# Performance work log

Hardware: AMD Instinct MI355X
Metric: run time of the kernel (lower is better)

The kernel has to match this reference:

```python
import jax, jax.numpy as jnp
import numpy as np

B, S, DIM, H, HD = 4, 1024, 1280, 16, 80
SCALE = HD ** -0.5
ROPE_THETA = 10000.0


def rotate_half(x):
    x1, x2 = jnp.split(x, 2, axis=-1)
    return jnp.concatenate([-x2, x1], axis=-1)


def setup_inputs() -> dict:
    key = jax.random.key(0)
    ks = jax.random.split(key, 5)
    x = jax.random.normal(ks[0], (B, S, DIM), dtype=jnp.float32)
    Wqkv = jax.random.normal(ks[1], (DIM, 3 * DIM), dtype=jnp.float32) * 0.02
    bqkv = jax.random.normal(ks[2], (3 * DIM,), dtype=jnp.float32) * 0.01
    Wproj = jax.random.normal(ks[3], (DIM, DIM), dtype=jnp.float32) * 0.02
    bproj = jax.random.normal(ks[4], (DIM,), dtype=jnp.float32) * 0.01
    # realistic rotary tables: (S, HD) with duplicated freq halves (matches rotate_half layout)
    inv_freq = 1.0 / (ROPE_THETA ** (jnp.arange(0, HD, 2, dtype=jnp.float32) / HD))
    freqs = jnp.outer(jnp.arange(S, dtype=jnp.float32), inv_freq)  # (S, HD/2)
    emb = jnp.concatenate([freqs, freqs], axis=-1)  # (S, HD)
    rope_cos = jnp.cos(emb)
    rope_sin = jnp.sin(emb)
    return {"x": x, "rope_cos": rope_cos, "rope_sin": rope_sin,
            "Wqkv": Wqkv, "bqkv": bqkv, "Wproj": Wproj, "bproj": bproj}


def reference(x, rope_cos, rope_sin, Wqkv, bqkv, Wproj, bproj):
    b, s, d = x.shape
    qkv = (x @ Wqkv + bqkv).reshape(b, s, 3, H, HD)
    q, k, v = qkv[:, :, 0], qkv[:, :, 1], qkv[:, :, 2]  # each (b, s, H, HD)
    cos = rope_cos[None, :, None, :]  # (1, s, 1, HD)
    sin = rope_sin[None, :, None, :]
    q = q * cos + rotate_half(q) * sin
    k = k * cos + rotate_half(k) * sin
    # SDPA with all-ones mask (full attention)
    scores = jnp.einsum("bqhd,bkhd->bhqk", q, k) * SCALE
    probs = jax.nn.softmax(scores, axis=-1)
    out = jnp.einsum("bhqk,bkhd->bqhd", probs, v).reshape(b, s, d)
    return out @ Wproj + bproj
```

## Files before the change

kernel.cpp:

```cpp
#include <hip/hip_runtime.h>
#include <math.h>

#define SCALE_F 0.11180339887498949f
#define HDP 96

typedef short  short8  __attribute__((ext_vector_type(8)));
typedef short  short4v __attribute__((ext_vector_type(4)));
typedef float  f32x4   __attribute__((ext_vector_type(4)));
typedef __bf16 bf16x8  __attribute__((ext_vector_type(8)));

__device__ __forceinline__ float bf2f(short s) {
  union { unsigned u; float f; } v;
  v.u = ((unsigned)(unsigned short)s) << 16;
  return v.f;
}
__device__ __forceinline__ short f2b(float f) {
  __bf16 h = (__bf16)f;
  return __builtin_bit_cast(short, h);
}
__device__ __forceinline__ bool probe_is_bf16(const unsigned* probe) {
  return (probe[1] & 0xFFFFu) != 0u;
}
__device__ __forceinline__ float load_scalar(const void* p, int i, bool isb) {
  return isb ? bf2f(((const short*)p)[i]) : ((const float*)p)[i];
}

__device__ __forceinline__ void gload_lds16(const short* g, short* l) {
  __builtin_amdgcn_global_load_lds(
      (const __attribute__((address_space(1))) void*)g,
      (__attribute__((address_space(3))) void*)l, 16, 0, 0);
}

template <typename V>
__device__ __forceinline__ auto mfma_try(V a, V b, f32x4 c, int)
    -> decltype(__builtin_amdgcn_mfma_f32_16x16x32_bf16(a, b, c, 0, 0, 0)) {
  return __builtin_amdgcn_mfma_f32_16x16x32_bf16(a, b, c, 0, 0, 0);
}
template <typename V>
__device__ __forceinline__ f32x4 mfma_try(V a, V b, f32x4 c, long) {
  return __builtin_amdgcn_mfma_f32_16x16x32_bf16(
      __builtin_bit_cast(bf16x8, a), __builtin_bit_cast(bf16x8, b), c, 0, 0, 0);
}
__device__ __forceinline__ f32x4 MFMA(short8 a, short8 b, f32x4 c) {
  return mfma_try(a, b, c, 0);
}

__global__ __launch_bounds__(256) void cvt_x_kernel(
    const void* __restrict__ xin, short* __restrict__ xout,
    const unsigned* __restrict__ probe) {
  bool isb = probe_is_bf16(probe);
  size_t i = ((size_t)blockIdx.x * 256 + threadIdx.x) * 8;
  if (isb) {
    *(short8*)&xout[i] = *(const short8*)((const short*)xin + i);
  } else {
    const float* f = (const float*)xin + i;
    float4 a0 = *(const float4*)f;
    float4 a1 = *(const float4*)(f + 4);
    short8 sv;
    sv[0] = f2b(a0.x); sv[1] = f2b(a0.y); sv[2] = f2b(a0.z); sv[3] = f2b(a0.w);
    sv[4] = f2b(a1.x); sv[5] = f2b(a1.y); sv[6] = f2b(a1.z); sv[7] = f2b(a1.w);
    *(short8*)&xout[i] = sv;
  }
}

__global__ __launch_bounds__(256) void transpose_kernel(
    const void* __restrict__ in, short* __restrict__ out, int R, int C,
    const unsigned* __restrict__ probe) {
  bool isb = probe_is_bf16(probe);
  __shared__ float tile[32][33];
  int t = threadIdx.x;
  int bx = blockIdx.x;
  int by = blockIdx.y;
  int r = t >> 3, c4 = (t & 7) * 4;
  size_t idx = (size_t)(by * 32 + r) * C + bx * 32 + c4;
  if (isb) {
    short4v v = *(const short4v*)((const short*)in + idx);
    tile[r][c4 + 0] = bf2f(v[0]);
    tile[r][c4 + 1] = bf2f(v[1]);
    tile[r][c4 + 2] = bf2f(v[2]);
    tile[r][c4 + 3] = bf2f(v[3]);
  } else {
    float4 v = *(const float4*)((const float*)in + idx);
    tile[r][c4 + 0] = v.x;
    tile[r][c4 + 1] = v.y;
    tile[r][c4 + 2] = v.z;
    tile[r][c4 + 3] = v.w;
  }
  __syncthreads();
  int rr = t >> 3, k4 = (t & 7) * 4;
  short4v o;
  o[0] = f2b(tile[k4 + 0][rr]);
  o[1] = f2b(tile[k4 + 1][rr]);
  o[2] = f2b(tile[k4 + 2][rr]);
  o[3] = f2b(tile[k4 + 3][rr]);
  *(short4v*)&out[(size_t)(bx * 32 + rr) * R + by * 32 + k4] = o;
}

__global__ __launch_bounds__(512, 2) void gemm_qkv_kernel(
    const short* __restrict__ X, const short* __restrict__ Wt,
    const void* __restrict__ bias, const unsigned* __restrict__ probe,
    short* __restrict__ Qw, short* __restrict__ Kw, short* __restrict__ Vt) {
  const int K = 1280;
  __shared__ short Al[2][2][8192];
  __shared__ short Bl[2][2][8192];
  int t = threadIdx.x;
  int bm = blockIdx.x / 15, bn = blockIdx.x % 15;
  int m0 = bm * 256, n0 = bn * 256;
  int w = t >> 6, lane = t & 63;
  int quad = lane >> 4, l16 = lane & 15, l8 = l16 & 7;
  int arow = (w >> 2) * 64 + l16;
  int brow = (w & 3) * 32 + l16;
  int sr = t >> 3, t8s = t * 8;
  int sjs = (t & 7) ^ (sr & 7);
  int soff0 = ((quad ^ l8) * 8);
  int soff1 = (((4 + quad) ^ l8) * 8);
  f32x4 acc[2][2][4][2] = {};

#define STAGE8(PTR, R0, KOFF, LP)                                            \
  {                                                                          \
    const short* g_ = (PTR) + (size_t)((R0) + sr) * 1280 + (KOFF) + sjs * 8; \
    gload_lds16(g_, (LP) + t8s);                                             \
    gload_lds16(g_ + 64 * 1280, (LP) + t8s + 4096);                          \
  }

#define PHASE(S, HA, HB, QM, QN, STAGE_CODE, DO_VW)                          \
  {                                                                          \
    short8 af[4][2], bfv[2][2];                                              \
    _Pragma("unroll") for (int mt = 0; mt < 4; mt++) {                       \
      int rp_ = (arow + mt * 16) * 64;                                       \
      af[mt][0] = *(const short8*)&Al[S][HA][rp_ + soff0];                   \
      af[mt][1] = *(const short8*)&Al[S][HA][rp_ + soff1];                   \
    }                                                                        \
    _Pragma("unroll") for (int nt = 0; nt < 2; nt++) {                       \
      int rp_ = (brow + nt * 16) * 64;                                       \
      bfv[nt][0] = *(const short8*)&Bl[S][HB][rp_ + soff0];                  \
      bfv[nt][1] = *(const short8*)&Bl[S][HB][rp_ + soff1];                  \
    }                                                                        \
    STAGE_CODE;                                                              \
    asm volatile("s_waitcnt lgkmcnt(0)" ::: "memory");                       \
    __builtin_amdgcn_sched_barrier(0);                                       \
    __builtin_amdgcn_s_setprio(1);                                           \
    _Pragma("unroll") for (int mt = 0; mt < 4; mt++)                         \
      _Pragma("unroll") for (int nt = 0; nt < 2; nt++) {                     \
        acc[QM][QN][mt][nt] = MFMA(af[mt][0], bfv[nt][0], acc[QM][QN][mt][nt]); \
        acc[QM][QN][mt][nt] = MFMA(af[mt][1], bfv[nt][1], acc[QM][QN][mt][nt]); \
      }                                                                      \
    __builtin_amdgcn_s_setprio(0);                                           \
    if (DO_VW) {                                                             \
      asm volatile("s_waitcnt vmcnt(4)" ::: "memory");                       \
      __builtin_amdgcn_sched_barrier(0);                                     \
    }                                                                        \
    __builtin_amdgcn_s_barrier();                                            \
  }

  STAGE8(X,  m0,       0,  &Al[0][0][0]);
  STAGE8(X,  m0 + 128, 0,  &Al[0][1][0]);
  STAGE8(Wt, n0,       0,  &Bl[0][0][0]);
  STAGE8(Wt, n0 + 128, 0,  &Bl[0][1][0]);
  STAGE8(X,  m0,       64, &Al[1][0][0]);
  STAGE8(Wt, n0,       64, &Bl[1][0][0]);
  asm volatile("s_waitcnt vmcnt(4)" ::: "memory");
  __builtin_amdgcn_sched_barrier(0);
  __builtin_amdgcn_s_barrier();

  for (int i = 0; i < 10; i++) {
    int k1 = (2 * i + 1) * 64;
    int k2 = (2 * i + 2) * 64; if (k2 >= K) k2 = 0;
    int k3 = (2 * i + 3) * 64; if (k3 >= K) k3 = 0;
    PHASE(0, 0, 0, 0, 0, STAGE8(X,  m0 + 128, k1, &Al[1][1][0]), 0);
    PHASE(0, 0, 1, 0, 1, STAGE8(Wt, n0 + 128, k1, &Bl[1][1][0]), 0);
    PHASE(0, 1, 0, 1, 0, STAGE8(X,  m0,       k2, &Al[0][0][0]), 0);
    PHASE(0, 1, 1, 1, 1, STAGE8(Wt, n0,       k2, &Bl[0][0][0]), 1);
    PHASE(1, 0, 0, 0, 0, STAGE8(X,  m0 + 128, k2, &Al[0][1][0]), 0);
    PHASE(1, 0, 1, 0, 1, STAGE8(Wt, n0 + 128, k2, &Bl[0][1][0]), 0);
    PHASE(1, 1, 0, 1, 0, STAGE8(X,  m0,       k3, &Al[1][0][0]), 0);
    PHASE(1, 1, 1, 1, 1, STAGE8(Wt, n0,       k3, &Bl[1][0][0]), 1);
  }
  asm volatile("s_waitcnt vmcnt(0)" ::: "memory");
  __builtin_amdgcn_sched_barrier(0);

  bool isb = probe_is_bf16(probe);
  float bv[2][2];
#pragma unroll
  for (int qn = 0; qn < 2; qn++)
#pragma unroll
    for (int nt = 0; nt < 2; nt++)
      bv[qn][nt] =
          load_scalar(bias, n0 + qn * 128 + (w & 3) * 32 + nt * 16 + l16, isb);
#pragma unroll
  for (int qm = 0; qm < 2; qm++)
#pragma unroll
    for (int mt = 0; mt < 4; mt++) {
      int mbase = m0 + qm * 128 + (w >> 2) * 64 + mt * 16 + quad * 4;
      int b = mbase >> 10, sbase = mbase & 1023;
#pragma unroll
      for (int qn = 0; qn < 2; qn++)
#pragma unroll
        for (int nt = 0; nt < 2; nt++) {
          int n = n0 + qn * 128 + (w & 3) * 32 + nt * 16 + l16;
          int which = n / 1280;
          int rmod = n - which * 1280;
          int h = rmod / 80;
          int d = rmod - h * 80;
          int bh = b * 16 + h;
          if (which == 2) {
            short4v vv;
#pragma unroll
            for (int reg = 0; reg < 4; reg++)
              vv[reg] = f2b(acc[qm][qn][mt][nt][reg] + bv[qn][nt]);
            *(short4v*)&Vt[((size_t)bh * 80 + d) * 1024 + sbase] = vv;
          } else {
            short* dst = (which == 0 ? Qw : Kw);
#pragma unroll
            for (int reg = 0; reg < 4; reg++)
              dst[((size_t)bh * 1024 + sbase + reg) * HDP + d] =
                  f2b(acc[qm][qn][mt][nt][reg] + bv[qn][nt]);
          }
        }
    }
#undef PHASE
#undef STAGE8
}

__global__ __launch_bounds__(256) void rope_kernel(
    short* __restrict__ Qw, short* __restrict__ Kw,
    const void* __restrict__ cosb, const void* __restrict__ sinb,
    const unsigned* __restrict__ probe) {
  bool isb = probe_is_bf16(probe);
  int t = threadIdx.x;
  int w = t >> 6, lane = t & 63;
  int job = blockIdx.x * 4 + w;
  int which = job & 1;
  int row = job >> 1;
  int s = row & 1023;
  short* ptr = (which ? Kw : Qw) + (size_t)row * HDP;
  float scale = which ? 1.0f : SCALE_F;
  if (lane < 40) {
    float p0 = bf2f(ptr[lane]);
    float p1 = bf2f(ptr[lane + 40]);
    float c0 = load_scalar(cosb, s * 80 + lane, isb);
    float s0 = load_scalar(sinb, s * 80 + lane, isb);
    float c1 = load_scalar(cosb, s * 80 + lane + 40, isb);
    float s1 = load_scalar(sinb, s * 80 + lane + 40, isb);
    ptr[lane] = f2b((p0 * c0 - p1 * s0) * scale);
    ptr[lane + 40] = f2b((p1 * c1 + p0 * s1) * scale);
  } else if (lane < 56) {
    ptr[40 + lane] = 0;
  }
}

__global__ __launch_bounds__(512, 4) void attn_kernel(
    const short* __restrict__ Qw, const short* __restrict__ Kw,
    const short* __restrict__ Vt, short* __restrict__ out) {
  __shared__ short Klds[2][64 * 104];
  __shared__ short Vlds[2][80 * 72];
  __shared__ short Ps[8][16 * 72];
  int t = threadIdx.x;
  int w = t >> 6, lane = t & 63;
  int quad = lane >> 4, l16 = lane & 15;
  int bh = blockIdx.x & 63;
  int qt = blockIdx.x >> 6;
  int q0 = qt * 128;
  const short* Kb = Kw + (size_t)bh * 1024 * HDP;
  const short* Vb = Vt + (size_t)bh * 80 * 1024;

  short8 aq[3];
  {
    const short* qrow = Qw + ((size_t)bh * 1024 + q0 + w * 16 + l16) * HDP;
#pragma unroll
    for (int ks = 0; ks < 3; ks++)
      aq[ks] = *(const short8*)&qrow[ks * 32 + quad * 8];
  }

  short8 kreg[2], vreg[2];
#define PREFETCH(c)                                                        \
  {                                                                        \
    {                                                                      \
      int row = t / 12, col = (t % 12) * 8;                                \
      kreg[0] = *(const short8*)&Kb[(size_t)((c) + row) * HDP + col];      \
    }                                                                      \
    if (t < 256) {                                                         \
      int idx = 512 + t;                                                   \
      int row = idx / 12, col = (idx % 12) * 8;                            \
      kreg[1] = *(const short8*)&Kb[(size_t)((c) + row) * HDP + col];      \
    }                                                                      \
    {                                                                      \
      int d = t >> 3, s0 = (t & 7) * 8;                                    \
      vreg[0] = *(const short8*)&Vb[(size_t)d * 1024 + (c) + s0];          \
    }                                                                      \
    if (t < 128) {                                                         \
      int idx = 512 + t;                                                   \
      int d = idx >> 3, s0 = (idx & 7) * 8;                                \
      vreg[1] = *(const short8*)&Vb[(size_t)d * 1024 + (c) + s0];          \
    }                                                                      \
  }
#define STORE_LDS(P)                                                       \
  {                                                                        \
    {                                                                      \
      int row = t / 12, col = (t % 12) * 8;                                \
      *(short8*)&Klds[P][row * 104 + col] = kreg[0];                       \
    }                                                                      \
    if (t < 256) {                                                         \
      int idx = 512 + t;                                                   \
      int row = idx / 12, col = (idx % 12) * 8;                            \
      *(short8*)&Klds[P][row * 104 + col] = kreg[1];                       \
    }                                                                      \
    {                                                                      \
      int d = t >> 3, s0 = (t & 7) * 8;                                    \
      *(short8*)&Vlds[P][d * 72 + s0] = vreg[0];                           \
    }                                                                      \
    if (t < 128) {                                                         \
      int idx = 512 + t;                                                   \
      int d = idx >> 3, s0 = (idx & 7) * 8;                                \
      *(short8*)&Vlds[P][d * 72 + s0] = vreg[1];                           \
    }                                                                      \
  }

  PREFETCH(0);
  STORE_LDS(0);
  __syncthreads();

  f32x4 ofr[5] = {};
  float lsum[4] = {0.f, 0.f, 0.f, 0.f};
  short* Pw = &Ps[w][0];

  int p = 0;
  for (int c = 0; c < 1024; c += 64, p ^= 1) {
    if (c + 64 < 1024) PREFETCH(c + 64);
    const short* Kl = &Klds[p][0];
    const short* Vl = &Vlds[p][0];
    f32x4 sf[4] = {};
#pragma unroll
    for (int nt = 0; nt < 4; nt++) {
      short8 bk0 = *(const short8*)&Kl[(nt * 16 + l16) * 104 + 0 * 32 + quad * 8];
      short8 bk1 = *(const short8*)&Kl[(nt * 16 + l16) * 104 + 1 * 32 + quad * 8];
      short8 bk2 = *(const short8*)&Kl[(nt * 16 + l16) * 104 + 2 * 32 + quad * 8];
      sf[nt] = MFMA(aq[0], bk0, sf[nt]);
      sf[nt] = MFMA(aq[1], bk1, sf[nt]);
      sf[nt] = MFMA(aq[2], bk2, sf[nt]);
    }
#pragma unroll
    for (int r = 0; r < 4; r++) {
      float p0 = __expf(fminf(sf[0][r], 30.f));
      float p1 = __expf(fminf(sf[1][r], 30.f));
      float p2 = __expf(fminf(sf[2][r], 30.f));
      float p3 = __expf(fminf(sf[3][r], 30.f));
      sf[0][r] = p0; sf[1][r] = p1; sf[2][r] = p2; sf[3][r] = p3;
      lsum[r] += (p0 + p1) + (p2 + p3);
    }
#pragma unroll
    for (int nt = 0; nt < 4; nt++)
#pragma unroll
      for (int r = 0; r < 4; r++)
        Pw[(quad * 4 + r) * 72 + nt * 16 + l16] = f2b(sf[nt][r]);
    __threadfence_block();
    short8 ap[2];
#pragma unroll
    for (int ks = 0; ks < 2; ks++)
      ap[ks] = *(const short8*)&Pw[l16 * 72 + ks * 32 + quad * 8];
#pragma unroll
    for (int nt = 0; nt < 5; nt++) {
      short8 bv0 = *(const short8*)&Vl[(nt * 16 + l16) * 72 + 0 * 32 + quad * 8];
      short8 bv1 = *(const short8*)&Vl[(nt * 16 + l16) * 72 + 1 * 32 + quad * 8];
      ofr[nt] = MFMA(ap[0], bv0, ofr[nt]);
      ofr[nt] = MFMA(ap[1], bv1, ofr[nt]);
    }
    if (c + 64 < 1024) {
      STORE_LDS(p ^ 1);
      __syncthreads();
    }
  }
#pragma unroll
  for (int off = 1; off < 16; off <<= 1)
#pragma unroll
    for (int r = 0; r < 4; r++) lsum[r] += __shfl_xor(lsum[r], off);
  float inv[4];
#pragma unroll
  for (int r = 0; r < 4; r++) inv[r] = 1.f / lsum[r];
  int b = bh >> 4, h = bh & 15;
#pragma unroll
  for (int nt = 0; nt < 5; nt++) {
    int d = nt * 16 + l16;
#pragma unroll
    for (int r = 0; r < 4; r++) {
      int s = q0 + w * 16 + quad * 4 + r;
      out[((size_t)(b * 1024 + s)) * 1280 + h * 80 + d] = f2b(ofr[nt][r] * inv[r]);
    }
  }
}

__global__ __launch_bounds__(256) void gemm_proj_kernel(
    const short* __restrict__ A, const short* __restrict__ Wt,
    const void* __restrict__ bias, const unsigned* __restrict__ probe,
    float* __restrict__ out) {
  const int K = 1280;
  __shared__ short As[2][128 * 32];
  __shared__ short Bs[2][128 * 32];
  int t = threadIdx.x;
  int bm = blockIdx.x / 10;
  int bn = blockIdx.x % 10;
  int m0 = bm * 128, n0 = bn * 128;
  int w = t >> 6, lane = t & 63;
  int wm = w & 1, wn = w >> 1;
  int quad = lane >> 4, l16 = lane & 15;
  int row = t >> 2, ch = (t & 3) * 8, row2 = row + 64;
  int t8 = t * 8;
  const short* Ar  = A  + (size_t)(m0 + row)  * K + ch;
  const short* Ar2 = A  + (size_t)(m0 + row2) * K + ch;
  const short* Wr  = Wt + (size_t)(n0 + row)  * K + ch;
  const short* Wr2 = Wt + (size_t)(n0 + row2) * K + ch;
  f32x4 acc[4][4] = {};
  gload_lds16(Ar,  &As[0][t8]);
  gload_lds16(Ar2, &As[0][t8 + 2048]);
  gload_lds16(Wr,  &Bs[0][t8]);
  gload_lds16(Wr2, &Bs[0][t8 + 2048]);
  __syncthreads();
  int p = 0;
#define PROJ_COMPUTE(pp)                                                      \
  {                                                                           \
    short8 af[4], bfr[4];                                                     \
    _Pragma("unroll") for (int mt = 0; mt < 4; mt++)                          \
        af[mt] = *(const short8*)&As[pp][(wm * 64 + mt * 16 + l16) * 32 + quad * 8]; \
    _Pragma("unroll") for (int nt = 0; nt < 4; nt++)                          \
        bfr[nt] = *(const short8*)&Bs[pp][(wn * 64 + nt * 16 + l16) * 32 + quad * 8]; \
    _Pragma("unroll") for (int mt = 0; mt < 4; mt++)                          \
        _Pragma("unroll") for (int nt = 0; nt < 4; nt++)                      \
            acc[mt][nt] = MFMA(af[mt], bfr[nt], acc[mt][nt]);                 \
  }
  for (int k0 = 32; k0 < K; k0 += 32, p ^= 1) {
    gload_lds16(Ar + k0,  &As[p ^ 1][t8]);
    gload_lds16(Ar2 + k0, &As[p ^ 1][t8 + 2048]);
    gload_lds16(Wr + k0,  &Bs[p ^ 1][t8]);
    gload_lds16(Wr2 + k0, &Bs[p ^ 1][t8 + 2048]);
    PROJ_COMPUTE(p);
    __syncthreads();
  }
  PROJ_COMPUTE(p);
  bool isb = probe_is_bf16(probe);
  float bv[4];
#pragma unroll
  for (int nt = 0; nt < 4; nt++)
    bv[nt] = load_scalar(bias, n0 + wn * 64 + nt * 16 + l16, isb);
#pragma unroll
  for (int mt = 0; mt < 4; mt++) {
#pragma unroll
    for (int nt = 0; nt < 4; nt++) {
      int n = n0 + wn * 64 + nt * 16 + l16;
#pragma unroll
      for (int reg = 0; reg < 4; reg++) {
        int m = m0 + wm * 64 + mt * 16 + quad * 4 + reg;
        out[(size_t)m * 1280 + n] = acc[mt][nt][reg] + bv[nt];
      }
    }
  }
}

extern "C" void kernel_launch(void* const* d_in, const int* in_sizes, int n_in,
                              void* d_out, int out_size, void* d_ws, size_t ws_size,
                              hipStream_t stream) {
  const void* x        = d_in[0];
  const void* rope_cos = d_in[1];
  const void* rope_sin = d_in[2];
  const void* Wqkv     = d_in[3];
  const void* bqkv     = d_in[4];
  const void* Wproj    = d_in[5];
  const void* bproj    = d_in[6];
  const unsigned* probe = (const unsigned*)rope_cos;
  char* ws = (char*)d_ws;
  short* Wt1 = (short*)(ws + 0);
  short* Wt2 = (short*)(ws + 9830400);
  short* Qw  = (short*)(ws + 13107200);
  short* Kw  = (short*)(ws + 25690112);
  short* Vt  = (short*)(ws + 38273024);
  short* Xb  = (short*)(ws + 48758784);
  short* At  = (short*)(ws + 48758784);

  cvt_x_kernel<<<2560, 256, 0, stream>>>(x, Xb, probe);
  transpose_kernel<<<dim3(3840 / 32, 1280 / 32), 256, 0, stream>>>(Wqkv, Wt1, 1280, 3840, probe);
  transpose_kernel<<<dim3(1280 / 32, 1280 / 32), 256, 0, stream>>>(Wproj, Wt2, 1280, 1280, probe);
  gemm_qkv_kernel<<<240, 512, 0, stream>>>(Xb, Wt1, bqkv, probe, Qw, Kw, Vt);
  rope_kernel<<<32768, 256, 0, stream>>>(Qw, Kw, rope_cos, rope_sin, probe);
  attn_kernel<<<512, 512, 0, stream>>>(Qw, Kw, Vt, At);
  gemm_proj_kernel<<<32 * 10, 256, 0, stream>>>(At, Wt2, bproj, probe, (float*)d_out);
}
```

Baseline: 242.7 us.

## Restructure QKV GEMM into 4-stage k32 pipeline with 128x64 warp tiles

Replaces the quadrant-phased double-buffered K=64 main loop of the QKV GEMM with a 4-deep ring of K=32 stages. Each iteration prefetches three tiles ahead, and each warp computes a contiguous 128x64 sub-tile with 32 MFMAs per barrier. The aim is fewer barriers per MFMA and deeper latency hiding of global loads into LDS. It also changes the LDS swizzle and the warp-to-output mapping. The trade-off is less work between barriers per K-step and a different LDS access pattern, which may raise bank conflicts.

```diff
diff --git a/kernel.cpp b/kernel.cpp
--- a/kernel.cpp
+++ b/kernel.cpp
@@ -100,126 +100,102 @@
     const short* __restrict__ X, const short* __restrict__ Wt,
     const void* __restrict__ bias, const unsigned* __restrict__ probe,
     short* __restrict__ Qw, short* __restrict__ Kw, short* __restrict__ Vt) {
-  const int K = 1280;
-  __shared__ short Al[2][2][8192];
-  __shared__ short Bl[2][2][8192];
+  __shared__ short Asl[4][8192];
+  __shared__ short Bsl[4][8192];
   int t = threadIdx.x;
   int bm = blockIdx.x / 15, bn = blockIdx.x % 15;
   int m0 = bm * 256, n0 = bn * 256;
   int w = t >> 6, lane = t & 63;
-  int quad = lane >> 4, l16 = lane & 15, l8 = l16 & 7;
-  int arow = (w >> 2) * 64 + l16;
-  int brow = (w & 3) * 32 + l16;
-  int sr = t >> 3, t8s = t * 8;
-  int sjs = (t & 7) ^ (sr & 7);
-  int soff0 = ((quad ^ l8) * 8);
-  int soff1 = (((4 + quad) ^ l8) * 8);
-  f32x4 acc[2][2][4][2] = {};
-
-#define STAGE8(PTR, R0, KOFF, LP)                                            \
+  int quad = lane >> 4, l16 = lane & 15;
+  int wm = w >> 2, wn = w & 3;
+  int arow = wm * 128 + l16;
+  int brow = wn * 64 + l16;
+  int qsw8 = (quad ^ ((l16 >> 1) & 3)) * 8;
+  int srow = t >> 2, t8s = t * 8;
+  int sks = (t & 3) ^ ((srow >> 1) & 3);
+  f32x4 acc[8][4] = {};
+
+#define STAGE32(KT)                                                          \
   {                                                                          \
-    const short* g_ = (PTR) + (size_t)((R0) + sr) * 1280 + (KOFF) + sjs * 8; \
-    gload_lds16(g_, (LP) + t8s);                                             \
-    gload_lds16(g_ + 64 * 1280, (LP) + t8s + 4096);                          \
-  }
-
-#define PHASE(S, HA, HB, QM, QN, STAGE_CODE, DO_VW)                          \
-  {                                                                          \
-    short8 af[4][2], bfv[2][2];                                              \
-    _Pragma("unroll") for (int mt = 0; mt < 4; mt++) {                       \
-      int rp_ = (arow + mt * 16) * 64;                                       \
-      af[mt][0] = *(const short8*)&Al[S][HA][rp_ + soff0];                   \
-      af[mt][1] = *(const short8*)&Al[S][HA][rp_ + soff1];                   \
-    }                                                                        \
-    _Pragma("unroll") for (int nt = 0; nt < 2; nt++) {                       \
-      int rp_ = (brow + nt * 16) * 64;                                       \
-      bfv[nt][0] = *(const short8*)&Bl[S][HB][rp_ + soff0];                  \
-      bfv[nt][1] = *(const short8*)&Bl[S][HB][rp_ + soff1];                  \
-    }                                                                        \
-    STAGE_CODE;                                                              \
-    asm volatile("s_waitcnt lgkmcnt(0)" ::: "memory");                       \
-    __builtin_amdgcn_sched_barrier(0);                                       \
-    __builtin_amdgcn_s_setprio(1);                                           \
-    _Pragma("unroll") for (int mt = 0; mt < 4; mt++)                         \
-      _Pragma("unroll") for (int nt = 0; nt < 2; nt++) {                     \
-        acc[QM][QN][mt][nt] = MFMA(af[mt][0], bfv[nt][0], acc[QM][QN][mt][nt]); \
-        acc[QM][QN][mt][nt] = MFMA(af[mt][1], bfv[nt][1], acc[QM][QN][mt][nt]); \
-      }                                                                      \
-    __builtin_amdgcn_s_setprio(0);                                           \
-    if (DO_VW) {                                                             \
-      asm volatile("s_waitcnt vmcnt(4)" ::: "memory");                       \
-      __builtin_amdgcn_sched_barrier(0);                                     \
-    }                                                                        \
-    __builtin_amdgcn_s_barrier();                                            \
-  }
-
-  STAGE8(X,  m0,       0,  &Al[0][0][0]);
-  STAGE8(X,  m0 + 128, 0,  &Al[0][1][0]);
-  STAGE8(Wt, n0,       0,  &Bl[0][0][0]);
-  STAGE8(Wt, n0 + 128, 0,  &Bl[0][1][0]);
-  STAGE8(X,  m0,       64, &Al[1][0][0]);
-  STAGE8(Wt, n0,       64, &Bl[1][0][0]);
-  asm volatile("s_waitcnt vmcnt(4)" ::: "memory");
+    int kn_ = (KT);                                                          \
+    int koff_ = (kn_ < 40) ? kn_ * 32 : 0;         \
+    int Sd_ = kn_ & 3;                                                       \
+    const short* ga_ = X + (size_t)(m0 + srow) * 1280 + koff_ + sks * 8;     \
+    gload_lds16(ga_, &Asl[Sd_][t8s]);                                        \
+    gload_lds16(ga_ + 128 * 1280, &Asl[Sd_][t8s + 4096]);                    \
+    const short* gb_ = Wt + (size_t)(n0 + srow) * 1280 + koff_ + sks * 8;    \
+    gload_lds16(gb_, &Bsl[Sd_][t8s]);                                        \
+    gload_lds16(gb_ + 128 * 1280, &Bsl[Sd_][t8s + 4096]);                    \
+  }
+
+  STAGE32(0);
+  STAGE32(1);
+  STAGE32(2);
+  asm volatile("s_waitcnt vmcnt(8)" ::: "memory");
   __builtin_amdgcn_sched_barrier(0);
   __builtin_amdgcn_s_barrier();
 
-  for (int i = 0; i < 10; i++) {
-    int k1 = (2 * i + 1) * 64;
-    int k2 = (2 * i + 2) * 64; if (k2 >= K) k2 = 0;
-    int k3 = (2 * i + 3) * 64; if (k3 >= K) k3 = 0;
-    PHASE(0, 0, 0, 0, 0, STAGE8(X,  m0 + 128, k1, &Al[1][1][0]), 0);
-    PHASE(0, 0, 1, 0, 1, STAGE8(Wt, n0 + 128, k1, &Bl[1][1][0]), 0);
-    PHASE(0, 1, 0, 1, 0, STAGE8(X,  m0,       k2, &Al[0][0][0]), 0);
-    PHASE(0, 1, 1, 1, 1, STAGE8(Wt, n0,       k2, &Bl[0][0][0]), 1);
-    PHASE(1, 0, 0, 0, 0, STAGE8(X,  m0 + 128, k2, &Al[0][1][0]), 0);
-    PHASE(1, 0, 1, 0, 1, STAGE8(Wt, n0 + 128, k2, &Bl[0][1][0]), 0);
-    PHASE(1, 1, 0, 1, 0, STAGE8(X,  m0,       k3, &Al[1][0][0]), 0);
-    PHASE(1, 1, 1, 1, 1, STAGE8(Wt, n0,       k3, &Bl[1][0][0]), 1);
+  for (int kt = 0; kt < 40; kt++) {
+    int S = kt & 3;
+    const short* As = &Asl[S][0];
+    const short* Bs = &Bsl[S][0];
+    STAGE32(kt + 3);
+    short8 af[8], bfv[4];
+#pragma unroll
+    for (int mt = 0; mt < 8; mt++)
+      af[mt] = *(const short8*)&As[(arow + mt * 16) * 32 + qsw8];
+#pragma unroll
+    for (int nt = 0; nt < 4; nt++)
+      bfv[nt] = *(const short8*)&Bs[(brow + nt * 16) * 32 + qsw8];
+    asm volatile("s_waitcnt lgkmcnt(0)" ::: "memory");
+    __builtin_amdgcn_sched_barrier(0);
+    __builtin_amdgcn_s_setprio(1);
+#pragma unroll
+    for (int mt = 0; mt < 8; mt++)
+#pragma unroll
+      for (int nt = 0; nt < 4; nt++)
+        acc[mt][nt] = MFMA(af[mt], bfv[nt], acc[mt][nt]);
+    __builtin_amdgcn_s_setprio(0);
+    asm volatile("s_waitcnt vmcnt(8)" ::: "memory");
+    __builtin_amdgcn_sched_barrier(0);
+    __builtin_amdgcn_s_barrier();
   }
   asm volatile("s_waitcnt vmcnt(0)" ::: "memory");
   __builtin_amdgcn_sched_barrier(0);
 
   bool isb = probe_is_bf16(probe);
-  float bv[2][2];
-#pragma unroll
-  for (int qn = 0; qn < 2; qn++)
-#pragma unroll
-    for (int nt = 0; nt < 2; nt++)
-      bv[qn][nt] =
-          load_scalar(bias, n0 + qn * 128 + (w & 3) * 32 + nt * 16 + l16, isb);
-#pragma unroll
-  for (int qm = 0; qm < 2; qm++)
-#pragma unroll
-    for (int mt = 0; mt < 4; mt++) {
-      int mbase = m0 + qm * 128 + (w >> 2) * 64 + mt * 16 + quad * 4;
-      int b = mbase >> 10, sbase = mbase & 1023;
-#pragma unroll
-      for (int qn = 0; qn < 2; qn++)
-#pragma unroll
-        for (int nt = 0; nt < 2; nt++) {
-          int n = n0 + qn * 128 + (w & 3) * 32 + nt * 16 + l16;
-          int which = n / 1280;
-          int rmod = n - which * 1280;
-          int h = rmod / 80;
-          int d = rmod - h * 80;
-          int bh = b * 16 + h;
-          if (which == 2) {
-            short4v vv;
-#pragma unroll
-            for (int reg = 0; reg < 4; reg++)
-              vv[reg] = f2b(acc[qm][qn][mt][nt][reg] + bv[qn][nt]);
-            *(short4v*)&Vt[((size_t)bh * 80 + d) * 1024 + sbase] = vv;
-          } else {
-            short* dst = (which == 0 ? Qw : Kw);
-#pragma unroll
-            for (int reg = 0; reg < 4; reg++)
-              dst[((size_t)bh * 1024 + sbase + reg) * HDP + d] =
-                  f2b(acc[qm][qn][mt][nt][reg] + bv[qn][nt]);
-          }
-        }
-    }
-#undef PHASE
-#undef STAGE8
+  float bv[4];
+#pragma unroll
+  for (int nt = 0; nt < 4; nt++)
+    bv[nt] = load_scalar(bias, n0 + wn * 64 + nt * 16 + l16, isb);
+#pragma unroll
+  for (int mt = 0; mt < 8; mt++) {
+    int mbase = m0 + wm * 128 + mt * 16 + quad * 4;
+    int b = mbase >> 10, sbase = mbase & 1023;
+#pragma unroll
+    for (int nt = 0; nt < 4; nt++) {
+      int n = n0 + wn * 64 + nt * 16 + l16;
+      int which = n / 1280;
+      int rmod = n - which * 1280;
+      int h = rmod / 80;
+      int d = rmod - h * 80;
+      int bh = b * 16 + h;
+      if (which == 2) {
+        short4v vv;
+#pragma unroll
+        for (int reg = 0; reg < 4; reg++)
+          vv[reg] = f2b(acc[mt][nt][reg] + bv[nt]);
+        *(short4v*)&Vt[((size_t)bh * 80 + d) * 1024 + sbase] = vv;
+      } else {
+        short* dst = (which == 0 ? Qw : Kw);
+#pragma unroll
+        for (int reg = 0; reg < 4; reg++)
+          dst[((size_t)bh * 1024 + sbase + reg) * HDP + d] =
+              f2b(acc[mt][nt][reg] + bv[nt]);
+      }
+    }
+  }
+#undef STAGE32
 }
 
 __global__ __launch_bounds__(256) void rope_kernel(
```

New measurement: 253.8 us. 4.6% more time.
